# Kernel tuning notes

Measured on AMD Instinct MI355X. Metric: run time of the kernel, lower is better.

## Reference

```python
import jax, jax.numpy as jnp
import numpy as np

TEMPERATURE = 0.1
LOSS_SCALE = 1.0
LAMBD = 0.5


def setup_inputs() -> dict:
    key = jax.random.key(0)
    k1, k2 = jax.random.split(key)
    B, D = 4096, 768
    predicted = jax.random.normal(k1, (B, D), dtype=jnp.float32)
    target = jax.random.normal(k2, (B, D), dtype=jnp.float32)
    return {"predicted": predicted, "target": target}


def reference(predicted, target):
    predicted = predicted.astype(jnp.float32)
    target = target.astype(jnp.float32)
    B = predicted.shape[0]

    # Pairwise L2 distances via Gram identity (avoids B x B x D intermediate):
    # ||p_i - t_j||^2 = ||p_i||^2 + ||t_j||^2 - 2 p_i . t_j
    p_sq = jnp.sum(predicted * predicted, axis=-1)  # [B]
    t_sq = jnp.sum(target * target, axis=-1)        # [B]
    cross = predicted @ target.T                    # [B, B]
    sq_dist = p_sq[:, None] + t_sq[None, :] - 2.0 * cross
    distances = jnp.sqrt(jnp.maximum(sq_dist, 0.0))  # [B, B]

    logits = -distances / TEMPERATURE
    # cross-entropy with labels = arange(B): mean of -log_softmax diagonal
    log_probs = jax.nn.log_softmax(logits, axis=-1)
    contrastive_dist_loss = -jnp.mean(jnp.diagonal(log_probs))

    # normalized L1 magnitude loss
    elementwise_l1 = jnp.sum(jnp.abs(predicted - target), axis=-1)  # [B]
    target_magnitude = jnp.sum(jnp.abs(target), axis=-1)            # [B]
    norm_factor = jax.lax.stop_gradient(target_magnitude)
    normalized_magnitude_loss = jnp.mean(elementwise_l1 / norm_factor)

    total_loss = LOSS_SCALE * (
        LAMBD * contrastive_dist_loss + (1.0 - LAMBD) * normalized_magnitude_loss
    )
    return (total_loss, contrastive_dist_loss, normalized_magnitude_loss)
```

## Files before the change

### kernel.cpp

```cpp
#include <hip/hip_runtime.h>
#include <hip/hip_bf16.h>
#include <math.h>

#define B_ROWS 4096
#define D_DIM  768

#define BM 128
#define BN 128
#define BK 64
#define NKT (D_DIM / BK)

typedef __attribute__((ext_vector_type(8))) short bf16x8;
typedef __attribute__((ext_vector_type(4))) float f32x4;

__device__ __forceinline__ unsigned short f32_to_bf16(float x) {
    unsigned int u = __float_as_uint(x);
    return (unsigned short)((u + 0x7fffu + ((u >> 16) & 1u)) >> 16);
}

__device__ __forceinline__ void async_copy16(const unsigned short* g, unsigned short* l) {
    __builtin_amdgcn_global_load_lds(
        (const __attribute__((address_space(1))) unsigned int*)g,
        (__attribute__((address_space(3))) unsigned int*)l,
        16, 0, 0);
}

__global__ void __launch_bounds__(256) rowstats_kernel(
    const float* __restrict__ P, const float* __restrict__ T,
    unsigned short* __restrict__ Pb, unsigned short* __restrict__ Tb,
    float* __restrict__ p_sq, float* __restrict__ t_sq,
    float* __restrict__ diagl, float* __restrict__ magr,
    float* __restrict__ rowsum)
{
    const int wave = threadIdx.x >> 6, lane = threadIdx.x & 63;
    const int i = blockIdx.x * 4 + wave;
    const f32x4* prow = (const f32x4*)(P + (size_t)i * D_DIM);
    const f32x4* trow = (const f32x4*)(T + (size_t)i * D_DIM);
    ushort4* pbrow = (ushort4*)(Pb + (size_t)i * D_DIM);
    ushort4* tbrow = (ushort4*)(Tb + (size_t)i * D_DIM);

    float psq = 0.f, tsq = 0.f, cr = 0.f, l1 = 0.f, tm = 0.f;
    #pragma unroll
    for (int u = 0; u < 3; ++u) {
        const int c4 = u * 64 + lane;
        f32x4 p = prow[c4], t = trow[c4];
        #pragma unroll
        for (int k = 0; k < 4; ++k) {
            psq += p[k] * p[k]; tsq += t[k] * t[k]; cr += p[k] * t[k];
            l1 += fabsf(p[k] - t[k]); tm += fabsf(t[k]);
        }
        pbrow[c4] = make_ushort4(f32_to_bf16(p[0]), f32_to_bf16(p[1]),
                                 f32_to_bf16(p[2]), f32_to_bf16(p[3]));
        tbrow[c4] = make_ushort4(f32_to_bf16(t[0]), f32_to_bf16(t[1]),
                                 f32_to_bf16(t[2]), f32_to_bf16(t[3]));
    }
    #pragma unroll
    for (int m = 1; m < 64; m <<= 1) {
        psq += __shfl_xor(psq, m, 64);
        tsq += __shfl_xor(tsq, m, 64);
        cr  += __shfl_xor(cr,  m, 64);
        l1  += __shfl_xor(l1,  m, 64);
        tm  += __shfl_xor(tm,  m, 64);
    }
    if (lane == 0) {
        p_sq[i] = psq;
        t_sq[i] = tsq;
        float sq = fmaxf(psq + tsq - 2.0f * cr, 0.0f);
        diagl[i] = -sqrtf(sq) * 10.0f;
        magr[i]  = l1 / tm;
        rowsum[i] = 0.0f;
    }
}

__global__ void __launch_bounds__(256) lse_gemm_kernel(
    const unsigned short* __restrict__ Pb, const unsigned short* __restrict__ Tb,
    const float* __restrict__ p_sq, const float* __restrict__ t_sq,
    const float* __restrict__ diagl, float* __restrict__ rowsum)
{
    __shared__ __align__(16) unsigned short As[2][BM * BK];
    __shared__ __align__(16) unsigned short Bs[2][BN * BK];

    const int tid = threadIdx.x;

    const int flat = blockIdx.y * (B_ROWS / BN) + blockIdx.x;
    const int xcd  = flat & 7;
    const int s    = flat >> 3;
    const int g    = xcd + ((s >> 6) << 3);
    const int w    = s & 63;
    const int i0   = (((g >> 2) << 3) + (w >> 3)) * BM;
    const int j0   = (((g & 3) << 3) + (w & 7)) * BN;

    const int lane  = tid & 63;
    const int wave  = tid >> 6;
    const int wm    = wave >> 1, wn = wave & 1;
    const int row16 = lane & 15, quad = lane >> 4;
    const int m_base = wm * 64, n_base = wn * 64;

    const int lrow   = lane >> 3;
    const int lchunk = (lane & 7) ^ lrow;
    const int swz = (quad ^ (row16 & 7)) << 4;

    const unsigned short* pg[4];
    const unsigned short* tg[4];
    #pragma unroll
    for (int it = 0; it < 4; ++it) {
        const int r = wave * 32 + it * 8 + lrow;
        pg[it] = Pb + (size_t)(i0 + r) * D_DIM + lchunk * 8;
        tg[it] = Tb + (size_t)(j0 + r) * D_DIM + lchunk * 8;
    }

    f32x4 acc[4][4];
    #pragma unroll
    for (int a = 0; a < 4; ++a)
        #pragma unroll
        for (int b = 0; b < 4; ++b)
            acc[a][b] = (f32x4){0.f, 0.f, 0.f, 0.f};

    #pragma unroll
    for (int it = 0; it < 4; ++it) {
        async_copy16(pg[it], &As[0][(wave * 4 + it) * 512]);
        async_copy16(tg[it], &Bs[0][(wave * 4 + it) * 512]);
    }

    for (int ktile = 0; ktile < NKT; ++ktile) {
        const int sel = ktile & 1;
        __syncthreads();

        if (ktile + 1 < NKT) {
            const int kt1 = (ktile + 1) * BK;
            #pragma unroll
            for (int it = 0; it < 4; ++it) {
                async_copy16(pg[it] + kt1, &As[sel ^ 1][(wave * 4 + it) * 512]);
                async_copy16(tg[it] + kt1, &Bs[sel ^ 1][(wave * 4 + it) * 512]);
            }
        }

        const char* Ab = (const char*)As[sel];
        const char* Bb = (const char*)Bs[sel];
        #pragma unroll
        for (int ks = 0; ks < BK; ks += 32) {
            const int kx = ks ? 64 : 0;
            bf16x8 a[4], b[4];
            #pragma unroll
            for (int mt = 0; mt < 4; ++mt) {
                const int off = (m_base + mt * 16 + row16) * 128 + swz;
                a[mt] = *(const bf16x8*)(Ab + (off ^ kx));
            }
            #pragma unroll
            for (int nt = 0; nt < 4; ++nt) {
                const int off = (n_base + nt * 16 + row16) * 128 + swz;
                b[nt] = *(const bf16x8*)(Bb + (off ^ kx));
            }
            #pragma unroll
            for (int mt = 0; mt < 4; ++mt)
                #pragma unroll
                for (int nt = 0; nt < 4; ++nt)
                    acc[mt][nt] = __builtin_amdgcn_mfma_f32_16x16x32_bf16(
                        a[mt], b[nt], acc[mt][nt], 0, 0, 0);
        }
    }

    const float NT_LOG2E = -14.4269504089f;
    const float LOG2E    = 1.44269504089f;
    float tsq_l[4];
    #pragma unroll
    for (int nt = 0; nt < 4; ++nt)
        tsq_l[nt] = t_sq[j0 + n_base + nt * 16 + row16];

    #pragma unroll
    for (int mt = 0; mt < 4; ++mt) {
        #pragma unroll
        for (int r = 0; r < 4; ++r) {
            const int i = i0 + m_base + mt * 16 + quad * 4 + r;
            const float psq = p_sq[i];
            const float c0  = -diagl[i] * LOG2E;
            float sfin = 0.f;
            #pragma unroll
            for (int nt = 0; nt < 4; ++nt) {
                float c  = acc[mt][nt][r];
                float sq = fmaxf(fmaf(-2.0f, c, psq + tsq_l[nt]), 0.0f);
                float d  = sqrtf(sq);
                float y  = fmaf(d, NT_LOG2E, c0);
                sfin += exp2f(y);
            }
            #pragma unroll
            for (int m = 1; m < 16; m <<= 1) sfin += __shfl_xor(sfin, m, 64);
            if (row16 == 0) atomicAdd(&rowsum[i], sfin);
        }
    }
}

__global__ void __launch_bounds__(256) finalize_kernel(
    const float* __restrict__ rowsum, const float* __restrict__ magr,
    float* __restrict__ out)
{
    const int tid = threadIdx.x;
    double sc = 0.0, sm = 0.0;
    for (int i = tid; i < B_ROWS; i += 256) {
        sc += log((double)rowsum[i]);
        sm += (double)magr[i];
    }
    #pragma unroll
    for (int m = 1; m < 64; m <<= 1) {
        sc += __shfl_xor(sc, m, 64);
        sm += __shfl_xor(sm, m, 64);
    }
    __shared__ double red[4][2];
    const int wave = tid >> 6, lane = tid & 63;
    if (lane == 0) { red[wave][0] = sc; red[wave][1] = sm; }
    __syncthreads();
    if (tid == 0) {
        sc = red[0][0] + red[1][0] + red[2][0] + red[3][0];
        sm = red[0][1] + red[1][1] + red[2][1] + red[3][1];
        double lc = sc / (double)B_ROWS;
        double lm = sm / (double)B_ROWS;
        out[0] = (float)(0.5 * lc + 0.5 * lm);
        out[1] = (float)lc;
        out[2] = (float)lm;
    }
}

extern "C" void kernel_launch(void* const* d_in, const int* in_sizes, int n_in,
                              void* d_out, int out_size, void* d_ws, size_t ws_size,
                              hipStream_t stream) {
    const float* P = (const float*)d_in[0];
    const float* T = (const float*)d_in[1];
    float* out = (float*)d_out;

    char* ws = (char*)d_ws;
    float* rowsum = (float*)ws;               ws += B_ROWS * sizeof(float);
    float* p_sq   = (float*)ws;               ws += B_ROWS * sizeof(float);
    float* t_sq   = (float*)ws;               ws += B_ROWS * sizeof(float);
    float* diagl  = (float*)ws;               ws += B_ROWS * sizeof(float);
    float* magr   = (float*)ws;               ws += B_ROWS * sizeof(float);
    unsigned short* Pb = (unsigned short*)ws; ws += (size_t)B_ROWS * D_DIM * 2;
    unsigned short* Tb = (unsigned short*)ws;

    rowstats_kernel<<<B_ROWS / 4, 256, 0, stream>>>(
        P, T, Pb, Tb, p_sq, t_sq, diagl, magr, rowsum);
    lse_gemm_kernel<<<dim3(B_ROWS / BN, B_ROWS / BM), 256, 0, stream>>>(
        Pb, Tb, p_sq, t_sq, diagl, rowsum);
    finalize_kernel<<<1, 256, 0, stream>>>(rowsum, magr, out);
}
```

Measured before the change: 131.8 us.

## Use 256x256 tiles with 512 threads and a 4-stage async LDS pipeline

The fused distance/logsumexp GEMM moves from 128x128 tiles with 256 threads and double buffering to 256x256 tiles with 512 threads (8 waves). It uses a 4-deep ring of BK=32 LDS buffers, explicit vmcnt waits, a single barrier per k-step, and s_setprio around the MFMA block. Half the waves load P and half load T with a new XOR swizzle, and the XCD-aware tile mapping is redone for the 256-block grid. The intent is more reuse per loaded byte and better overlap of global loads with MFMA work. The cost is higher register pressure and only 256 blocks, which may leave compute units underfilled.

```diff
diff --git a/kernel.cpp b/kernel.cpp
--- a/kernel.cpp
+++ b/kernel.cpp
@@ -5,10 +5,11 @@
 #define B_ROWS 4096
 #define D_DIM  768
 
-#define BM 128
-#define BN 128
-#define BK 64
+#define BM 256
+#define BN 256
+#define BK 32
 #define NKT (D_DIM / BK)
+#define NBUF 4
 
 typedef __attribute__((ext_vector_type(8))) short bf16x8;
 typedef __attribute__((ext_vector_type(4))) float f32x4;
@@ -72,106 +73,118 @@
     }
 }
 
-__global__ void __launch_bounds__(256) lse_gemm_kernel(
+__global__ void __launch_bounds__(512, 2) lse_gemm_kernel(
     const unsigned short* __restrict__ Pb, const unsigned short* __restrict__ Tb,
     const float* __restrict__ p_sq, const float* __restrict__ t_sq,
     const float* __restrict__ diagl, float* __restrict__ rowsum)
 {
-    __shared__ __align__(16) unsigned short As[2][BM * BK];
-    __shared__ __align__(16) unsigned short Bs[2][BN * BK];
-
-    const int tid = threadIdx.x;
-
-    const int flat = blockIdx.y * (B_ROWS / BN) + blockIdx.x;
+    __shared__ __align__(16) unsigned short S[NBUF][2][BM * BK];
+
+    const int tid  = threadIdx.x;
+    const int lane = tid & 63, wave = tid >> 6;
+
+    const int flat = blockIdx.x;
     const int xcd  = flat & 7;
     const int s    = flat >> 3;
-    const int g    = xcd + ((s >> 6) << 3);
-    const int w    = s & 63;
-    const int i0   = (((g >> 2) << 3) + (w >> 3)) * BM;
-    const int j0   = (((g & 3) << 3) + (w & 7)) * BN;
-
-    const int lane  = tid & 63;
-    const int wave  = tid >> 6;
-    const int wm    = wave >> 1, wn = wave & 1;
+    const int ti   = ((xcd >> 1) << 2) + (s >> 3);
+    const int tj   = ((xcd & 1) << 3) + (s & 7);
+    const int i0   = ti * BM, j0 = tj * BN;
+
+    const int wm = wave >> 2, wn = wave & 3;
     const int row16 = lane & 15, quad = lane >> 4;
-    const int m_base = wm * 64, n_base = wn * 64;
-
-    const int lrow   = lane >> 3;
-    const int lchunk = (lane & 7) ^ lrow;
-    const int swz = (quad ^ (row16 & 7)) << 4;
-
-    const unsigned short* pg[4];
-    const unsigned short* tg[4];
-    #pragma unroll
-    for (int it = 0; it < 4; ++it) {
-        const int r = wave * 32 + it * 8 + lrow;
-        pg[it] = Pb + (size_t)(i0 + r) * D_DIM + lchunk * 8;
-        tg[it] = Tb + (size_t)(j0 + r) * D_DIM + lchunk * 8;
-    }
-
-    f32x4 acc[4][4];
-    #pragma unroll
-    for (int a = 0; a < 4; ++a)
+
+    int aoff[8], boff[4];
+    #pragma unroll
+    for (int mt = 0; mt < 8; ++mt) {
+        const int R = wm * 128 + mt * 16 + row16;
+        aoff[mt] = R * BK + ((quad ^ ((R >> 1) & 3)) << 3);
+    }
+    #pragma unroll
+    for (int nt = 0; nt < 4; ++nt) {
+        const int R = wn * 64 + nt * 16 + row16;
+        boff[nt] = R * BK + ((quad ^ ((R >> 1) & 3)) << 3);
+    }
+
+    const bool isB = wave >= 4;
+    const int  sw  = wave & 3;
+    const int  q   = lane & 3;
+    const unsigned short* gsrc = isB ? Tb : Pb;
+    const int  r0g = isB ? j0 : i0;
+    const unsigned short* gp[4];
+    int lbase[4];
+    #pragma unroll
+    for (int j = 0; j < 4; ++j) {
+        const int R = sw * 64 + j * 16 + (lane >> 2);
+        const int g = q ^ ((R >> 1) & 3);
+        gp[j] = gsrc + (size_t)(r0g + R) * D_DIM + g * 8;
+        lbase[j] = (sw * 64 + j * 16) * BK;
+    }
+
+    f32x4 acc[8][4];
+    #pragma unroll
+    for (int a = 0; a < 8; ++a)
         #pragma unroll
         for (int b = 0; b < 4; ++b)
             acc[a][b] = (f32x4){0.f, 0.f, 0.f, 0.f};
 
-    #pragma unroll
-    for (int it = 0; it < 4; ++it) {
-        async_copy16(pg[it], &As[0][(wave * 4 + it) * 512]);
-        async_copy16(tg[it], &Bs[0][(wave * 4 + it) * 512]);
-    }
-
-    for (int ktile = 0; ktile < NKT; ++ktile) {
-        const int sel = ktile & 1;
-        __syncthreads();
-
-        if (ktile + 1 < NKT) {
-            const int kt1 = (ktile + 1) * BK;
+    auto compute = [&](int buf) {
+        const unsigned short* Ab = &S[buf][0][0];
+        const unsigned short* Bb = &S[buf][1][0];
+        bf16x8 a[8], b[4];
+        #pragma unroll
+        for (int mt = 0; mt < 8; ++mt) a[mt] = *(const bf16x8*)(Ab + aoff[mt]);
+        #pragma unroll
+        for (int nt = 0; nt < 4; ++nt) b[nt] = *(const bf16x8*)(Bb + boff[nt]);
+        __builtin_amdgcn_s_setprio(1);
+        #pragma unroll
+        for (int mt = 0; mt < 8; ++mt)
             #pragma unroll
-            for (int it = 0; it < 4; ++it) {
-                async_copy16(pg[it] + kt1, &As[sel ^ 1][(wave * 4 + it) * 512]);
-                async_copy16(tg[it] + kt1, &Bs[sel ^ 1][(wave * 4 + it) * 512]);
-            }
-        }
-
-        const char* Ab = (const char*)As[sel];
-        const char* Bb = (const char*)Bs[sel];
-        #pragma unroll
-        for (int ks = 0; ks < BK; ks += 32) {
-            const int kx = ks ? 64 : 0;
-            bf16x8 a[4], b[4];
-            #pragma unroll
-            for (int mt = 0; mt < 4; ++mt) {
-                const int off = (m_base + mt * 16 + row16) * 128 + swz;
-                a[mt] = *(const bf16x8*)(Ab + (off ^ kx));
-            }
-            #pragma unroll
-            for (int nt = 0; nt < 4; ++nt) {
-                const int off = (n_base + nt * 16 + row16) * 128 + swz;
-                b[nt] = *(const bf16x8*)(Bb + (off ^ kx));
-            }
-            #pragma unroll
-            for (int mt = 0; mt < 4; ++mt)
-                #pragma unroll
-                for (int nt = 0; nt < 4; ++nt)
-                    acc[mt][nt] = __builtin_amdgcn_mfma_f32_16x16x32_bf16(
-                        a[mt], b[nt], acc[mt][nt], 0, 0, 0);
-        }
-    }
+            for (int nt = 0; nt < 4; ++nt)
+                acc[mt][nt] = __builtin_amdgcn_mfma_f32_16x16x32_bf16(
+                    a[mt], b[nt], acc[mt][nt], 0, 0, 0);
+        __builtin_amdgcn_s_setprio(0);
+    };
+
+    #pragma unroll
+    for (int t = 0; t < 3; ++t)
+        #pragma unroll
+        for (int j = 0; j < 4; ++j)
+            async_copy16(gp[j] + t * BK, &S[t][isB][lbase[j]]);
+    asm volatile("s_waitcnt vmcnt(8)" ::: "memory");
+    __builtin_amdgcn_s_barrier();
+
+    for (int t = 0; t < NKT - 3; ++t) {
+        const int pb = (t + 3) & 3;
+        #pragma unroll
+        for (int j = 0; j < 4; ++j)
+            async_copy16(gp[j] + (t + 3) * BK, &S[pb][isB][lbase[j]]);
+        compute(t & 3);
+        __builtin_amdgcn_sched_barrier(0);
+        asm volatile("s_waitcnt vmcnt(8) lgkmcnt(0)" ::: "memory");
+        __builtin_amdgcn_s_barrier();
+    }
+    compute(21 & 3);
+    __builtin_amdgcn_sched_barrier(0);
+    asm volatile("s_waitcnt vmcnt(4) lgkmcnt(0)" ::: "memory");
+    __builtin_amdgcn_s_barrier();
+    compute(22 & 3);
+    __builtin_amdgcn_sched_barrier(0);
+    asm volatile("s_waitcnt vmcnt(0) lgkmcnt(0)" ::: "memory");
+    __builtin_amdgcn_s_barrier();
+    compute(23 & 3);
 
     const float NT_LOG2E = -14.4269504089f;
     const float LOG2E    = 1.44269504089f;
     float tsq_l[4];
     #pragma unroll
     for (int nt = 0; nt < 4; ++nt)
-        tsq_l[nt] = t_sq[j0 + n_base + nt * 16 + row16];
-
-    #pragma unroll
-    for (int mt = 0; mt < 4; ++mt) {
+        tsq_l[nt] = t_sq[j0 + wn * 64 + nt * 16 + row16];
+
+    #pragma unroll
+    for (int mt = 0; mt < 8; ++mt) {
         #pragma unroll
         for (int r = 0; r < 4; ++r) {
-            const int i = i0 + m_base + mt * 16 + quad * 4 + r;
+            const int i = i0 + wm * 128 + mt * 16 + quad * 4 + r;
             const float psq = p_sq[i];
             const float c0  = -diagl[i] * LOG2E;
             float sfin = 0.f;
@@ -238,7 +251,7 @@
 
     rowstats_kernel<<<B_ROWS / 4, 256, 0, stream>>>(
         P, T, Pb, Tb, p_sq, t_sq, diagl, magr, rowsum);
-    lse_gemm_kernel<<<dim3(B_ROWS / BN, B_ROWS / BM), 256, 0, stream>>>(
+    lse_gemm_kernel<<<(B_ROWS / BM) * (B_ROWS / BN), 512, 0, stream>>>(
         Pb, Tb, p_sq, t_sq, diagl, rowsum);
     finalize_kernel<<<1, 256, 0, stream>>>(rowsum, magr, out);
 }
```

Result: faster. 126.3 us, median of 2 (-4.2%).
